# Performance work log

Measured on AMD Instinct MI355X. Metric: run time of the kernel, lower is better.

## Reference

```python
import jax, jax.numpy as jnp
import numpy as np

ALPHA = 0.025
BETA = 0.00025
V_TH = 1.0
EXP_TAU = 50.0          # tau_v / dt
T_NOW = 10.0            # current simulation step counter self.t
REFRAC_STEPS = 2        # refractory_period / dt
INV_TAU_V = float(np.exp(-1.0 / 50.0))   # exp(-dt/tau_v)
INV_TAU_I = float(np.exp(-1.0))          # exp(-dt/tau_i)
INV_TAU_V_PAIR = INV_TAU_V               # tau_v_pair defaults to tau_v
INV_TAU_I_PAIR = INV_TAU_I               # tau_i_pair defaults to tau_i

B, N = 32, 4096


def setup_inputs() -> dict:
    key = jax.random.key(0)
    ks = jax.random.split(key, 8)
    return {
        "inp": jax.random.normal(ks[0], (B, N), jnp.float32),
        "W_rec": jax.random.uniform(ks[1], (N, N), jnp.float32),  # nonneg dense adjacency weights
        "mem_pot": jax.random.normal(ks[2], (B, N), jnp.float32),
        "mem_cur": jax.random.normal(ks[3], (B, N), jnp.float32),
        "mem_pot_paired": jax.random.normal(ks[4], (B, N), jnp.float32),
        "mem_cur_paired": jax.random.normal(ks[5], (B, N), jnp.float32),
        "st": jnp.zeros((N,), jnp.float32),
        "refrac_neurons": jax.random.randint(ks[6], (B, N), 0, 3, jnp.int32),
    }


def reference(inp, W_rec, mem_pot, mem_cur, mem_pot_paired, mem_cur_paired, st, refrac_neurons):
    sign_mask = W_rec > 0  # torch: sign(W_rec) > 0 (weights are nonneg)

    # decrement refractory counters
    refrac = jnp.where(refrac_neurons > 0, refrac_neurons - 1, refrac_neurons)

    # threshold (ceil+clamp -> {0,1} spikes)
    S = jnp.clip(jnp.ceil(mem_pot - V_TH), 0.0, 1.0)                     # (B,N)
    S_paired = jnp.clip(jnp.ceil(mem_pot_paired - V_TH - ALPHA), 0.0, 1.0)

    # ---- plasticity weight update ----
    sp_max = S_paired.max(axis=0)            # (N,)
    st_new = jnp.where(S > 0, T_NOW, st)     # broadcasts (N,) -> (B,N), as in torch
    max_st = st_new.max(axis=0)              # (N,)
    # meshgrid(a,b) with ij indexing: |a-b|[i,j] = |max_st[i]-max_st[j]|
    diff = jnp.abs(max_st[:, None] - max_st[None, :])                    # (N,N)
    update_mask = (sp_max[:, None] > 0) & sign_mask                      # (N,N)
    updated = W_rec + BETA - jnp.where(update_mask,
                                       ALPHA * jnp.exp(diff / EXP_TAU),
                                       0.0)
    updated = jnp.clip(updated, 0.0, 1.0)
    W_new = jnp.where(sign_mask, updated, W_rec)

    # ---- integrate ----
    active = refrac == 0
    mem_cur_n = jnp.where(active, inp + S @ W_new + mem_cur, mem_cur)
    mem_cur_p_n = jnp.where(active, S @ W_new.T + mem_cur_paired, mem_cur_paired)
    mem_pot_n = jnp.where(active, mem_cur_n + mem_pot, mem_pot)
    mem_pot_p_n = jnp.where(active, mem_cur_p_n + mem_pot_paired, mem_pot_paired)

    # leak
    mem_pot_n = mem_pot_n * INV_TAU_V
    mem_cur_n = mem_cur_n * INV_TAU_I
    mem_pot_p_n = mem_pot_p_n * INV_TAU_V_PAIR
    mem_cur_p_n = mem_cur_p_n * INV_TAU_I_PAIR

    # reset spiked neurons
    mem_pot_n = jnp.where(S > 0, 0.0, mem_pot_n)
    mem_pot_p_n = jnp.where(S_paired > 0, 0.0, mem_pot_p_n)
    refrac_new = jnp.where(S > 0, REFRAC_STEPS, refrac)

    return S, mem_pot_n, W_new, mem_cur_n, mem_pot_p_n, mem_cur_p_n, refrac_new
```

## Files before the change

### kernel.cpp

```cpp
#include <hip/hip_runtime.h>
#include <cstdint>
#include <cstddef>

constexpr int N = 4096;
constexpr int B = 32;
constexpr int BN = B * N;
constexpr size_t NN = (size_t)N * N;
constexpr int KCHUNKS = 4;
constexpr int KC = N / KCHUNKS;

constexpr float ALPHA = 0.025f;
constexpr float BETA = 0.00025f;
constexpr float T_NOW = 10.0f;
constexpr float INV_EXP_TAU = 0.02f;
constexpr float INV_TAU_V = 0.98019867f;
constexpr float INV_TAU_I = 0.36787944f;

typedef __attribute__((ext_vector_type(8))) short short8;
typedef __attribute__((ext_vector_type(4))) float f32x4;

__device__ inline unsigned short f2bf(float f) {
  uint32_t u = __float_as_uint(f);
  u += 0x7FFFu + ((u >> 16) & 1u);
  return (unsigned short)(u >> 16);
}

__global__ __launch_bounds__(256) void pass_a(
    const float* __restrict__ mem_pot, const float* __restrict__ mem_pot_p,
    const float* __restrict__ st, float* __restrict__ S_out,
    unsigned short* __restrict__ S_bf,
    uint32_t* __restrict__ maskS, uint32_t* __restrict__ maskSP,
    float* __restrict__ max_st, float* __restrict__ rowfac) {
  int j = blockIdx.x * blockDim.x + threadIdx.x;
  if (j >= N) return;
  float stj = st[j];
  uint32_t ms = 0u, msp = 0u;
  float maxv = -3.0e38f;
  #pragma unroll
  for (int b = 0; b < B; ++b) {
    float p = mem_pot[b * N + j];
    float pp = mem_pot_p[b * N + j];
    bool s = (p - 1.0f) > 0.0f;
    bool sp = ((pp - 1.0f) - ALPHA) > 0.0f;
    S_out[b * N + j] = s ? 1.0f : 0.0f;
    S_bf[b * N + j] = s ? 0x3F80u : 0u;
    ms |= (uint32_t)s << b;
    msp |= (uint32_t)sp << b;
    maxv = fmaxf(maxv, s ? T_NOW : stj);
  }
  maskS[j] = ms;
  maskSP[j] = msp;
  max_st[j] = maxv;
  rowfac[j] = msp ? ALPHA : 0.0f;
}

__global__ __launch_bounds__(256) void pass_b(
    const float* __restrict__ W, const float* __restrict__ max_st,
    const float* __restrict__ rowfac, float* __restrict__ Wout) {
  int i = blockIdx.x;
  int tid = threadIdx.x;
  float mst_i = max_st[i];
  float fac_i = rowfac[i];

  const float4* __restrict__ Wrow = (const float4*)(W + (size_t)i * N);
  float4* __restrict__ Wo = (float4*)(Wout + (size_t)i * N);
  const float4* __restrict__ mstv = (const float4*)max_st;

  float4 w[4], mj[4];
  #pragma unroll
  for (int it = 0; it < 4; ++it) {
    int idx = it * 256 + tid;
    w[it] = Wrow[idx];
    mj[it] = mstv[idx];
  }

  auto upd = [&](float ww, float mstj) -> float {
    float d = fabsf(mst_i - mstj);
    float ex = __expf(d * INV_EXP_TAU);
    float u = ww + BETA - fac_i * ex;
    u = fminf(fmaxf(u, 0.0f), 1.0f);
    return (ww > 0.0f) ? u : ww;
  };

  #pragma unroll
  for (int it = 0; it < 4; ++it) {
    int idx = it * 256 + tid;
    float4 wo;
    wo.x = upd(w[it].x, mj[it].x);
    wo.y = upd(w[it].y, mj[it].y);
    wo.z = upd(w[it].z, mj[it].z);
    wo.w = upd(w[it].w, mj[it].w);
    Wo[idx] = wo;
  }
}

__global__ __launch_bounds__(256) void pass_mfma(
    const float* __restrict__ Wn, const unsigned short* __restrict__ S_bf,
    float* __restrict__ partSW, float* __restrict__ partSWT) {
  int wv = threadIdx.x >> 6;
  int lane = threadIdx.x & 63;
  int ntile = blockIdx.x * 4 + wv;
  int j0 = ntile * 16;
  int kchunk = blockIdx.y;
  int kbase = kchunk * KC;
  int gemm = blockIdx.z;
  int quad = lane >> 4;
  int nl = lane & 15;

  f32x4 acc0 = {0.f, 0.f, 0.f, 0.f};
  f32x4 acc1 = {0.f, 0.f, 0.f, 0.f};
  const unsigned short* A0p = S_bf + (size_t)nl * N;
  const unsigned short* A1p = S_bf + (size_t)(nl + 16) * N;

  if (gemm == 0) {
    #pragma unroll 4
    for (int it = 0; it < KC / 32; ++it) {
      int k0 = kbase + it * 32;
      short8 a0 = *(const short8*)(A0p + k0 + quad * 8);
      short8 a1 = *(const short8*)(A1p + k0 + quad * 8);
      short8 bf;
      #pragma unroll
      for (int i = 0; i < 8; ++i) {
        float f = Wn[(size_t)(k0 + quad * 8 + i) * N + j0 + nl];
        bf[i] = (short)f2bf(f);
      }
      acc0 = __builtin_amdgcn_mfma_f32_16x16x32_bf16(a0, bf, acc0, 0, 0, 0);
      acc1 = __builtin_amdgcn_mfma_f32_16x16x32_bf16(a1, bf, acc1, 0, 0, 0);
    }
  } else {
    const float4* __restrict__ Wr =
        (const float4*)(Wn + (size_t)(j0 + nl) * N);
    #pragma unroll 4
    for (int it = 0; it < KC / 32; ++it) {
      int k0 = kbase + it * 32;
      short8 a0 = *(const short8*)(A0p + k0 + quad * 8);
      short8 a1 = *(const short8*)(A1p + k0 + quad * 8);
      int f4 = (k0 + quad * 8) >> 2;
      float4 f0 = Wr[f4];
      float4 f1 = Wr[f4 + 1];
      short8 bf;
      bf[0] = (short)f2bf(f0.x); bf[1] = (short)f2bf(f0.y);
      bf[2] = (short)f2bf(f0.z); bf[3] = (short)f2bf(f0.w);
      bf[4] = (short)f2bf(f1.x); bf[5] = (short)f2bf(f1.y);
      bf[6] = (short)f2bf(f1.z); bf[7] = (short)f2bf(f1.w);
      acc0 = __builtin_amdgcn_mfma_f32_16x16x32_bf16(a0, bf, acc0, 0, 0, 0);
      acc1 = __builtin_amdgcn_mfma_f32_16x16x32_bf16(a1, bf, acc1, 0, 0, 0);
    }
  }

  float* part = (gemm == 0) ? partSW : partSWT;
  size_t base = (size_t)kchunk * BN + j0 + nl;
  #pragma unroll
  for (int r = 0; r < 4; ++r) {
    part[base + (size_t)(quad * 4 + r) * N] = acc0[r];
    part[base + (size_t)(16 + quad * 4 + r) * N] = acc1[r];
  }
}

__global__ __launch_bounds__(256) void pass_d(
    const float* __restrict__ inp, const float* __restrict__ mem_pot,
    const float* __restrict__ mem_cur, const float* __restrict__ mem_pot_p,
    const float* __restrict__ mem_cur_p, const int* __restrict__ refrac_in,
    const uint32_t* __restrict__ maskS, const uint32_t* __restrict__ maskSP,
    const float* __restrict__ partSW, const float* __restrict__ partSWT,
    float* __restrict__ pot_out, float* __restrict__ cur_out,
    float* __restrict__ potp_out, float* __restrict__ curp_out,
    float* __restrict__ refrac_out) {
  int e = blockIdx.x * 256 + threadIdx.x;
  int b = e >> 12;
  int j = e & (N - 1);

  float SW = 0.0f, SWT = 0.0f;
  #pragma unroll
  for (int c = 0; c < KCHUNKS; ++c) {
    SW += partSW[(size_t)c * BN + e];
    SWT += partSWT[(size_t)c * BN + e];
  }

  int r = refrac_in[e];
  int rd = (r > 0) ? (r - 1) : r;
  bool active = (rd == 0);
  bool s = (maskS[j] >> b) & 1u;
  bool sp = (maskSP[j] >> b) & 1u;
  float cur = mem_cur[e], pot = mem_pot[e];
  float curp = mem_cur_p[e], potp = mem_pot_p[e];

  float cur_n = active ? (inp[e] + SW + cur) : cur;
  float curp_n = active ? (SWT + curp) : curp;
  float pot_n = active ? (cur_n + pot) : pot;
  float potp_n = active ? (curp_n + potp) : potp;

  pot_n *= INV_TAU_V;
  cur_n *= INV_TAU_I;
  potp_n *= INV_TAU_V;
  curp_n *= INV_TAU_I;

  if (s) pot_n = 0.0f;
  if (sp) potp_n = 0.0f;
  int rn = s ? 2 : rd;

  pot_out[e] = pot_n;
  cur_out[e] = cur_n;
  potp_out[e] = potp_n;
  curp_out[e] = curp_n;
  refrac_out[e] = (float)rn;
}

extern "C" void kernel_launch(void* const* d_in, const int* in_sizes, int n_in,
                              void* d_out, int out_size, void* d_ws, size_t ws_size,
                              hipStream_t stream) {
  const float* inp = (const float*)d_in[0];
  const float* W = (const float*)d_in[1];
  const float* mem_pot = (const float*)d_in[2];
  const float* mem_cur = (const float*)d_in[3];
  const float* mem_pot_p = (const float*)d_in[4];
  const float* mem_cur_p = (const float*)d_in[5];
  const float* st = (const float*)d_in[6];
  const int* refrac = (const int*)d_in[7];

  float* out = (float*)d_out;
  float* S_out = out;
  float* pot_out = out + BN;
  float* W_out = out + 2 * (size_t)BN;
  float* cur_out = W_out + NN;
  float* potp_out = cur_out + BN;
  float* curp_out = potp_out + BN;
  float* refrac_out = curp_out + BN;

  uint32_t* maskS = (uint32_t*)d_ws;
  uint32_t* maskSP = maskS + N;
  float* max_st = (float*)(maskSP + N);
  float* rowfac = max_st + N;
  unsigned short* S_bf = (unsigned short*)(rowfac + N);
  float* partSW = (float*)(S_bf + BN);
  float* partSWT = partSW + (size_t)KCHUNKS * BN;

  pass_a<<<N / 256, 256, 0, stream>>>(mem_pot, mem_pot_p, st, S_out, S_bf,
                                      maskS, maskSP, max_st, rowfac);
  pass_b<<<N, 256, 0, stream>>>(W, max_st, rowfac, W_out);
  pass_mfma<<<dim3(64, KCHUNKS, 2), 256, 0, stream>>>(W_out, S_bf, partSW,
                                                      partSWT);
  pass_d<<<BN / 256, 256, 0, stream>>>(inp, mem_pot, mem_cur, mem_pot_p,
                                       mem_cur_p, refrac, maskS, maskSP,
                                       partSW, partSWT, pot_out, cur_out,
                                       potp_out, curp_out, refrac_out);
}
```

Baseline: 166.8 us.

## Fuse S@W^T MFMA into weight-update pass and split S@W into its own kernel

The weight-update kernel now also computes the S@W_new^T product. It converts each freshly updated row tile to bf16 and feeds it straight to MFMA, producing partial sums over 8 column chunks. This avoids re-reading W_new from memory for the transposed GEMM. The remaining S@W GEMM runs in a separate kernel with 8 K-chunks instead of 4, which adds more partial buffers for the final pass to reduce.

```diff
diff --git a/kernel.cpp b/kernel.cpp
--- a/kernel.cpp
+++ b/kernel.cpp
@@ -6,8 +6,11 @@
 constexpr int B = 32;
 constexpr int BN = B * N;
 constexpr size_t NN = (size_t)N * N;
-constexpr int KCHUNKS = 4;
-constexpr int KC = N / KCHUNKS;
+
+constexpr int JCH = 8;
+constexpr int JC = N / JCH;
+constexpr int KCH = 8;
+constexpr int KC = N / KCH;
 
 constexpr float ALPHA = 0.025f;
 constexpr float BETA = 0.00025f;
@@ -55,24 +58,25 @@
 }
 
 __global__ __launch_bounds__(256) void pass_b(
-    const float* __restrict__ W, const float* __restrict__ max_st,
-    const float* __restrict__ rowfac, float* __restrict__ Wout) {
-  int i = blockIdx.x;
-  int tid = threadIdx.x;
+    const float* __restrict__ W, const unsigned short* __restrict__ S_bf,
+    const float* __restrict__ max_st, const float* __restrict__ rowfac,
+    float* __restrict__ Wout, float* __restrict__ partSWT) {
+  int wv = threadIdx.x >> 6;
+  int lane = threadIdx.x & 63;
+  int nl = lane & 15;
+  int quad = lane >> 4;
+  int i = blockIdx.x * 64 + wv * 16 + nl;
+  int jc = blockIdx.y;
+
   float mst_i = max_st[i];
   float fac_i = rowfac[i];
-
-  const float4* __restrict__ Wrow = (const float4*)(W + (size_t)i * N);
-  float4* __restrict__ Wo = (float4*)(Wout + (size_t)i * N);
-  const float4* __restrict__ mstv = (const float4*)max_st;
-
-  float4 w[4], mj[4];
-  #pragma unroll
-  for (int it = 0; it < 4; ++it) {
-    int idx = it * 256 + tid;
-    w[it] = Wrow[idx];
-    mj[it] = mstv[idx];
-  }
+  const float* __restrict__ Wrow = W + (size_t)i * N;
+  float* __restrict__ WoRow = Wout + (size_t)i * N;
+  const unsigned short* __restrict__ A0p = S_bf + (size_t)nl * N;
+  const unsigned short* __restrict__ A1p = S_bf + (size_t)(nl + 16) * N;
+
+  f32x4 acc0 = {0.f, 0.f, 0.f, 0.f};
+  f32x4 acc1 = {0.f, 0.f, 0.f, 0.f};
 
   auto upd = [&](float ww, float mstj) -> float {
     float d = fabsf(mst_i - mstj);
@@ -82,78 +86,79 @@
     return (ww > 0.0f) ? u : ww;
   };
 
-  #pragma unroll
-  for (int it = 0; it < 4; ++it) {
-    int idx = it * 256 + tid;
-    float4 wo;
-    wo.x = upd(w[it].x, mj[it].x);
-    wo.y = upd(w[it].y, mj[it].y);
-    wo.z = upd(w[it].z, mj[it].z);
-    wo.w = upd(w[it].w, mj[it].w);
-    Wo[idx] = wo;
-  }
-}
-
-__global__ __launch_bounds__(256) void pass_mfma(
+  #pragma unroll 2
+  for (int it = 0; it < JC / 32; ++it) {
+    int j = jc * JC + it * 32 + quad * 8;
+    float4 w0 = *(const float4*)(Wrow + j);
+    float4 w1 = *(const float4*)(Wrow + j + 4);
+    float4 m0 = *(const float4*)(max_st + j);
+    float4 m1 = *(const float4*)(max_st + j + 4);
+    short8 a0 = *(const short8*)(A0p + j);
+    short8 a1 = *(const short8*)(A1p + j);
+
+    float4 o0, o1;
+    o0.x = upd(w0.x, m0.x); o0.y = upd(w0.y, m0.y);
+    o0.z = upd(w0.z, m0.z); o0.w = upd(w0.w, m0.w);
+    o1.x = upd(w1.x, m1.x); o1.y = upd(w1.y, m1.y);
+    o1.z = upd(w1.z, m1.z); o1.w = upd(w1.w, m1.w);
+    *(float4*)(WoRow + j) = o0;
+    *(float4*)(WoRow + j + 4) = o1;
+
+    short8 bf;
+    bf[0] = (short)f2bf(o0.x); bf[1] = (short)f2bf(o0.y);
+    bf[2] = (short)f2bf(o0.z); bf[3] = (short)f2bf(o0.w);
+    bf[4] = (short)f2bf(o1.x); bf[5] = (short)f2bf(o1.y);
+    bf[6] = (short)f2bf(o1.z); bf[7] = (short)f2bf(o1.w);
+
+    acc0 = __builtin_amdgcn_mfma_f32_16x16x32_bf16(a0, bf, acc0, 0, 0, 0);
+    acc1 = __builtin_amdgcn_mfma_f32_16x16x32_bf16(a1, bf, acc1, 0, 0, 0);
+  }
+
+  size_t base = (size_t)jc * BN + (size_t)(blockIdx.x * 64 + wv * 16 + nl);
+  #pragma unroll
+  for (int r = 0; r < 4; ++r) {
+    partSWT[base + (size_t)(quad * 4 + r) * N] = acc0[r];
+    partSWT[base + (size_t)(16 + quad * 4 + r) * N] = acc1[r];
+  }
+}
+
+__global__ __launch_bounds__(256) void pass_sw(
     const float* __restrict__ Wn, const unsigned short* __restrict__ S_bf,
-    float* __restrict__ partSW, float* __restrict__ partSWT) {
+    float* __restrict__ partSW) {
   int wv = threadIdx.x >> 6;
   int lane = threadIdx.x & 63;
   int ntile = blockIdx.x * 4 + wv;
   int j0 = ntile * 16;
   int kchunk = blockIdx.y;
   int kbase = kchunk * KC;
-  int gemm = blockIdx.z;
   int quad = lane >> 4;
   int nl = lane & 15;
 
   f32x4 acc0 = {0.f, 0.f, 0.f, 0.f};
   f32x4 acc1 = {0.f, 0.f, 0.f, 0.f};
-  const unsigned short* A0p = S_bf + (size_t)nl * N;
-  const unsigned short* A1p = S_bf + (size_t)(nl + 16) * N;
-
-  if (gemm == 0) {
-    #pragma unroll 4
-    for (int it = 0; it < KC / 32; ++it) {
-      int k0 = kbase + it * 32;
-      short8 a0 = *(const short8*)(A0p + k0 + quad * 8);
-      short8 a1 = *(const short8*)(A1p + k0 + quad * 8);
-      short8 bf;
-      #pragma unroll
-      for (int i = 0; i < 8; ++i) {
-        float f = Wn[(size_t)(k0 + quad * 8 + i) * N + j0 + nl];
-        bf[i] = (short)f2bf(f);
-      }
-      acc0 = __builtin_amdgcn_mfma_f32_16x16x32_bf16(a0, bf, acc0, 0, 0, 0);
-      acc1 = __builtin_amdgcn_mfma_f32_16x16x32_bf16(a1, bf, acc1, 0, 0, 0);
+  const unsigned short* __restrict__ A0p = S_bf + (size_t)nl * N;
+  const unsigned short* __restrict__ A1p = S_bf + (size_t)(nl + 16) * N;
+
+  #pragma unroll 4
+  for (int it = 0; it < KC / 32; ++it) {
+    int k0 = kbase + it * 32;
+    short8 a0 = *(const short8*)(A0p + k0 + quad * 8);
+    short8 a1 = *(const short8*)(A1p + k0 + quad * 8);
+    short8 bf;
+    #pragma unroll
+    for (int i = 0; i < 8; ++i) {
+      float f = Wn[(size_t)(k0 + quad * 8 + i) * N + j0 + nl];
+      bf[i] = (short)f2bf(f);
     }
-  } else {
-    const float4* __restrict__ Wr =
-        (const float4*)(Wn + (size_t)(j0 + nl) * N);
-    #pragma unroll 4
-    for (int it = 0; it < KC / 32; ++it) {
-      int k0 = kbase + it * 32;
-      short8 a0 = *(const short8*)(A0p + k0 + quad * 8);
-      short8 a1 = *(const short8*)(A1p + k0 + quad * 8);
-      int f4 = (k0 + quad * 8) >> 2;
-      float4 f0 = Wr[f4];
-      float4 f1 = Wr[f4 + 1];
-      short8 bf;
-      bf[0] = (short)f2bf(f0.x); bf[1] = (short)f2bf(f0.y);
-      bf[2] = (short)f2bf(f0.z); bf[3] = (short)f2bf(f0.w);
-      bf[4] = (short)f2bf(f1.x); bf[5] = (short)f2bf(f1.y);
-      bf[6] = (short)f2bf(f1.z); bf[7] = (short)f2bf(f1.w);
-      acc0 = __builtin_amdgcn_mfma_f32_16x16x32_bf16(a0, bf, acc0, 0, 0, 0);
-      acc1 = __builtin_amdgcn_mfma_f32_16x16x32_bf16(a1, bf, acc1, 0, 0, 0);
-    }
-  }
-
-  float* part = (gemm == 0) ? partSW : partSWT;
+    acc0 = __builtin_amdgcn_mfma_f32_16x16x32_bf16(a0, bf, acc0, 0, 0, 0);
+    acc1 = __builtin_amdgcn_mfma_f32_16x16x32_bf16(a1, bf, acc1, 0, 0, 0);
+  }
+
   size_t base = (size_t)kchunk * BN + j0 + nl;
   #pragma unroll
   for (int r = 0; r < 4; ++r) {
-    part[base + (size_t)(quad * 4 + r) * N] = acc0[r];
-    part[base + (size_t)(16 + quad * 4 + r) * N] = acc1[r];
+    partSW[base + (size_t)(quad * 4 + r) * N] = acc0[r];
+    partSW[base + (size_t)(16 + quad * 4 + r) * N] = acc1[r];
   }
 }
 
@@ -172,10 +177,9 @@
 
   float SW = 0.0f, SWT = 0.0f;
   #pragma unroll
-  for (int c = 0; c < KCHUNKS; ++c) {
-    SW += partSW[(size_t)c * BN + e];
-    SWT += partSWT[(size_t)c * BN + e];
-  }
+  for (int c = 0; c < KCH; ++c) SW += partSW[(size_t)c * BN + e];
+  #pragma unroll
+  for (int c = 0; c < JCH; ++c) SWT += partSWT[(size_t)c * BN + e];
 
   int r = refrac_in[e];
   int rd = (r > 0) ? (r - 1) : r;
@@ -233,13 +237,13 @@
   float* rowfac = max_st + N;
   unsigned short* S_bf = (unsigned short*)(rowfac + N);
   float* partSW = (float*)(S_bf + BN);
-  float* partSWT = partSW + (size_t)KCHUNKS * BN;
+  float* partSWT = partSW + (size_t)KCH * BN;
 
   pass_a<<<N / 256, 256, 0, stream>>>(mem_pot, mem_pot_p, st, S_out, S_bf,
                                       maskS, maskSP, max_st, rowfac);
-  pass_b<<<N, 256, 0, stream>>>(W, max_st, rowfac, W_out);
-  pass_mfma<<<dim3(64, KCHUNKS, 2), 256, 0, stream>>>(W_out, S_bf, partSW,
-                                                      partSWT);
+  pass_b<<<dim3(N / 64, JCH), 256, 0, stream>>>(W, S_bf, max_st, rowfac,
+                                                W_out, partSWT);
+  pass_sw<<<dim3(64, KCH), 256, 0, stream>>>(W_out, S_bf, partSW);
   pass_d<<<BN / 256, 256, 0, stream>>>(inp, mem_pot, mem_cur, mem_pot_p,
                                        mem_cur_p, refrac, maskS, maskSP,
                                        partSW, partSWT, pot_out, cur_out,
```

New measurement: 171.1 us. 2.5% more time.
